# Kernel tuning notes

Hardware: AMD Instinct MI355X
Metric: run time of the kernel (lower is better)

Reference implementation:

```python
import jax, jax.numpy as jnp
import numpy as np

T, H, N, D = 4096, 16, 16, 64


def setup_inputs() -> dict:
    key = jax.random.key(0)
    ks = jax.random.split(key, 8)
    x = jax.random.normal(ks[0], (T, H, D), dtype=jnp.float32)
    dt = jax.random.uniform(ks[1], (T, H), dtype=jnp.float32) * 0.1  # small positive timesteps
    B = jax.random.normal(ks[2], (T, H, N), dtype=jnp.float32)
    C = jax.random.normal(ks[3], (T, H, N), dtype=jnp.float32)
    mask = jax.random.randint(ks[4], (T,), 0, 2).astype(jnp.float32)  # reset flags in {0,1}
    initial_carry = jax.random.normal(ks[5], (H, N, D), dtype=jnp.float32)
    log_decay = jax.random.normal(ks[6], (H,), dtype=jnp.float32) * 0.1
    skip_weight = jnp.ones((H, D), dtype=jnp.float32)
    return {"x": x, "dt": dt, "B": B, "C": C, "mask": mask,
            "initial_carry": initial_carry, "log_decay": log_decay,
            "skip_weight": skip_weight}


def _binary_operator(q_i, q_j):
    # elementwise; broadcasting replaces the original per-time vmap
    a_i, b_i, c_i = q_i
    a_j, b_j, c_j = q_j
    a_out = a_j * a_i * (1.0 - c_j) + a_j * c_j
    b_out = (a_j * b_i + b_j) * (1.0 - c_j) + b_j * c_j
    c_out = c_i * (1.0 - c_j) + c_j
    return (a_out, b_out, c_out)


def reference(x, dt, B, C, mask, initial_carry, log_decay, skip_weight):
    num_heads = dt.shape[1]
    decay_rate = -jnp.exp(log_decay)                        # [H]
    decay_factor = jnp.exp(dt * decay_rate[None, :])        # [T,H]
    decay_factor = decay_factor[:, :, None, None]           # [T,H,1,1]
    decay_factor = jnp.concatenate(
        [jnp.ones((1, num_heads, 1, 1), dtype=decay_factor.dtype), decay_factor], axis=0)
    driving_input = jnp.einsum('th,thn,thd->thnd', dt, B, x)  # [T,H,N,D]
    driving_input = jnp.concatenate([initial_carry[None, ...], driving_input], axis=0)
    m = jnp.concatenate([jnp.zeros((1,), dtype=mask.dtype), mask])
    m = m[:, None, None, None]                              # [T+1,1,1,1]
    _, hidden_states, _ = jax.lax.associative_scan(
        _binary_operator, (decay_factor, driving_input, m))
    next_carry = hidden_states[-1]                          # [H,N,D]
    valid_states = hidden_states[1:]                        # [T,H,N,D]
    output = jnp.einsum('thn,thnd->thd', C, valid_states)   # [T,H,D]
    output = output + skip_weight[None, :, :] * x
    return (next_carry, output)
```

## Files before the change

### kernel.cpp

```cpp
#include <hip/hip_runtime.h>

#define T_LEN 4096
#define H 16
#define N 16
#define D 64
#define NC 256
#define CL (T_LEN / NC)
#define HND (H * N * D)

static __device__ __forceinline__ unsigned short f2bf(float f) {
    union { float f; unsigned u; } v; v.f = f;
    unsigned r = (v.u + 0x7fffu + ((v.u >> 16) & 1u)) >> 16;
    return (unsigned short)r;
}
static __device__ __forceinline__ float bf2f(unsigned short s) {
    union { unsigned u; float f; } v; v.u = ((unsigned)s) << 16;
    return v.f;
}

__global__ __launch_bounds__(64)
void k1_local(const float* __restrict__ x, const float* __restrict__ dt,
              const float* __restrict__ B, const float* __restrict__ C,
              const float* __restrict__ mask, const float* __restrict__ log_decay,
              const float* __restrict__ skip_weight,
              unsigned short* __restrict__ Lb, float* __restrict__ Pbuf,
              float* __restrict__ OL) {
    const int c = blockIdx.x, h = blockIdx.y;
    const int d = threadIdx.x;
    const float rate = -__expf(log_decay[h]);
    const int t0 = c * CL;

    __shared__ float Bs[CL * N], Cs[CL * N];
    {
        const float4* Bg = (const float4*)B;
        const float4* Cg = (const float4*)C;
        const int j = d;
        const int row = j >> 2, off = j & 3;
        const float dtv = dt[(t0 + row) * H + h];
        float4 bv = Bg[((t0 + row) * H + h) * (N / 4) + off];
        bv.x *= dtv; bv.y *= dtv; bv.z *= dtv; bv.w *= dtv;
        ((float4*)Bs)[j] = bv;
        ((float4*)Cs)[j] = Cg[((t0 + row) * H + h) * (N / 4) + off];
    }
    __syncthreads();

    float s[N];
#pragma unroll
    for (int n = 0; n < N; ++n) s[n] = 0.f;
    const float swv = skip_weight[h * D + d];
    float P = 1.f;

#pragma unroll
    for (int ss = 0; ss < CL; ++ss) {
        const int t = t0 + ss;
        const float dtv = dt[t * H + h];
        const float mv  = mask[t];
        const float a   = (1.f - mv) * __expf(dtv * rate);
        const float xv  = x[(t * H + h) * D + d];
        P *= a;
        float acc = swv * xv;
        const float4* Br4 = (const float4*)(Bs + ss * N);
        const float4* Cr4 = (const float4*)(Cs + ss * N);
#pragma unroll
        for (int q = 0; q < 4; ++q) {
            const float4 bv = Br4[q];
            const float4 cv = Cr4[q];
            s[4*q+0] = a * s[4*q+0] + bv.x * xv;  acc += cv.x * s[4*q+0];
            s[4*q+1] = a * s[4*q+1] + bv.y * xv;  acc += cv.y * s[4*q+1];
            s[4*q+2] = a * s[4*q+2] + bv.z * xv;  acc += cv.z * s[4*q+2];
            s[4*q+3] = a * s[4*q+3] + bv.w * xv;  acc += cv.w * s[4*q+3];
        }
        OL[(t * H + h) * D + d] = acc;
    }

    unsigned short* Lp = Lb + ((size_t)(c * H + h) * N) * D + d;
#pragma unroll
    for (int n = 0; n < N; ++n) Lp[n * D] = f2bf(s[n]);
    if (d == 0) Pbuf[h * NC + c] = P;
}

__global__ __launch_bounds__(256)
void k2_combine(const float* __restrict__ initial_carry,
                unsigned short* __restrict__ LE, const float* __restrict__ Pbuf,
                float* __restrict__ next_carry) {
    const int idx = blockIdx.x * 256 + threadIdx.x;
    const int h = blockIdx.x >> 2;
    float carry = initial_carry[idx];

#pragma unroll 1
    for (int r = 0; r < NC / 128; ++r) {
        float l[128];
#pragma unroll
        for (int k = 0; k < 128; ++k)
            l[k] = bf2f(LE[(size_t)(r * 128 + k) * HND + idx]);
#pragma unroll
        for (int k = 0; k < 128; ++k) {
            const float p = Pbuf[h * NC + r * 128 + k];
            LE[(size_t)(r * 128 + k) * HND + idx] = f2bf(carry);
            carry = p * carry + l[k];
        }
    }
    next_carry[idx] = carry;
}

__global__ __launch_bounds__(64)
void k3_correct(const float* __restrict__ dt, const float* __restrict__ C,
                const float* __restrict__ mask, const float* __restrict__ log_decay,
                const unsigned short* __restrict__ Eb,
                const float* __restrict__ OL, float* __restrict__ out) {
    const int c = blockIdx.x, h = blockIdx.y;
    const int d = threadIdx.x;
    const float rate = -__expf(log_decay[h]);
    const int t0 = c * CL;

    __shared__ float Cs[CL * N];
    {
        const float4* Cg = (const float4*)C;
        const int j = d;
        const int row = j >> 2, off = j & 3;
        ((float4*)Cs)[j] = Cg[((t0 + row) * H + h) * (N / 4) + off];
    }
    __syncthreads();

    float E[N];
    {
        const unsigned short* Ep = Eb + ((size_t)(c * H + h) * N) * D + d;
#pragma unroll
        for (int n = 0; n < N; ++n) E[n] = bf2f(Ep[n * D]);
    }

    float pa = 1.f;
#pragma unroll
    for (int ss = 0; ss < CL; ++ss) {
        const int t = t0 + ss;
        const float dtv = dt[t * H + h];
        const float mv  = mask[t];
        pa *= (1.f - mv) * __expf(dtv * rate);
        const float4* Cr4 = (const float4*)(Cs + ss * N);
        float corr = 0.f;
#pragma unroll
        for (int q = 0; q < 4; ++q) {
            const float4 cv = Cr4[q];
            corr += cv.x * E[4*q+0] + cv.y * E[4*q+1]
                  + cv.z * E[4*q+2] + cv.w * E[4*q+3];
        }
        const float ol = OL[(t * H + h) * D + d];
        __builtin_nontemporal_store(ol + pa * corr, &out[(t * H + h) * D + d]);
    }
}

extern "C" void kernel_launch(void* const* d_in, const int* in_sizes, int n_in,
                              void* d_out, int out_size, void* d_ws, size_t ws_size,
                              hipStream_t stream) {
    const float* x    = (const float*)d_in[0];
    const float* dt   = (const float*)d_in[1];
    const float* B    = (const float*)d_in[2];
    const float* C    = (const float*)d_in[3];
    const float* mask = (const float*)d_in[4];
    const float* ic   = (const float*)d_in[5];
    const float* ld   = (const float*)d_in[6];
    const float* sw   = (const float*)d_in[7];
    float* out = (float*)d_out;

    float* Pbuf = (float*)d_ws;
    unsigned short* Lb = (unsigned short*)((char*)d_ws + 16384);
    float* OL = (float*)((char*)d_ws + 16384 + (size_t)NC * HND * 2);

    dim3 grid(NC, H), block(64);
    k1_local<<<grid, block, 0, stream>>>(x, dt, B, C, mask, ld, sw, Lb, Pbuf, OL);
    k2_combine<<<dim3(HND / 256), dim3(256), 0, stream>>>(ic, Lb, Pbuf, out);
    k3_correct<<<grid, block, 0, stream>>>(dt, C, mask, ld, Lb, OL, out + HND);
}
```

Before: 38.71 us.

## Recompute chunk scan from carried state instead of storing local outputs

The first pass now only computes each chunk's end state and decay product, and no longer writes the full local output array. The third kernel reruns the chunk recurrence starting from the combined carry-in state and produces the final output directly. This removes a large intermediate write plus a later read, at the cost of repeating the state recurrence arithmetic. It also packs four chunks per 256-thread block and precomputes the decay factors once into a workspace buffer that both kernels share.

New measurement: 35.49 us. -8.3%, faster.

```diff
diff --git a/kernel.cpp b/kernel.cpp
--- a/kernel.cpp
+++ b/kernel.cpp
@@ -6,6 +6,7 @@
 #define D 64
 #define NC 256
 #define CL (T_LEN / NC)
+#define CPB 4
 #define HND (H * N * D)
 
 static __device__ __forceinline__ unsigned short f2bf(float f) {
@@ -18,59 +19,58 @@
     return v.f;
 }
 
-__global__ __launch_bounds__(64)
+__global__ __launch_bounds__(256)
 void k1_local(const float* __restrict__ x, const float* __restrict__ dt,
-              const float* __restrict__ B, const float* __restrict__ C,
-              const float* __restrict__ mask, const float* __restrict__ log_decay,
-              const float* __restrict__ skip_weight,
+              const float* __restrict__ B, const float* __restrict__ mask,
+              const float* __restrict__ log_decay,
               unsigned short* __restrict__ Lb, float* __restrict__ Pbuf,
-              float* __restrict__ OL) {
-    const int c = blockIdx.x, h = blockIdx.y;
-    const int d = threadIdx.x;
+              float* __restrict__ Abuf) {
+    const int cq = blockIdx.x, h = blockIdx.y;
+    const int tid = threadIdx.x;
+    const int w = tid >> 6, d = tid & 63;
+    const int c = cq * CPB + w;
+    const int t00 = cq * CPB * CL;
     const float rate = -__expf(log_decay[h]);
-    const int t0 = c * CL;
 
-    __shared__ float Bs[CL * N], Cs[CL * N];
+    __shared__ float Bs[CPB * CL * N];
+    __shared__ float As[CPB * CL];
     {
         const float4* Bg = (const float4*)B;
-        const float4* Cg = (const float4*)C;
-        const int j = d;
+        const int j = tid;
         const int row = j >> 2, off = j & 3;
-        const float dtv = dt[(t0 + row) * H + h];
-        float4 bv = Bg[((t0 + row) * H + h) * (N / 4) + off];
+        const int t = t00 + row;
+        const float dtv = dt[t * H + h];
+        float4 bv = Bg[(t * H + h) * (N / 4) + off];
         bv.x *= dtv; bv.y *= dtv; bv.z *= dtv; bv.w *= dtv;
         ((float4*)Bs)[j] = bv;
-        ((float4*)Cs)[j] = Cg[((t0 + row) * H + h) * (N / 4) + off];
+        if (off == 0) {
+            const float av = (1.f - mask[t]) * __expf(dtv * rate);
+            As[row] = av;
+            Abuf[h * T_LEN + t] = av;
+        }
     }
     __syncthreads();
 
     float s[N];
 #pragma unroll
     for (int n = 0; n < N; ++n) s[n] = 0.f;
-    const float swv = skip_weight[h * D + d];
     float P = 1.f;
+    const int t0 = c * CL;
 
 #pragma unroll
     for (int ss = 0; ss < CL; ++ss) {
-        const int t = t0 + ss;
-        const float dtv = dt[t * H + h];
-        const float mv  = mask[t];
-        const float a   = (1.f - mv) * __expf(dtv * rate);
-        const float xv  = x[(t * H + h) * D + d];
+        const float a  = As[w * CL + ss];
+        const float xv = x[((t0 + ss) * H + h) * D + d];
         P *= a;
-        float acc = swv * xv;
-        const float4* Br4 = (const float4*)(Bs + ss * N);
-        const float4* Cr4 = (const float4*)(Cs + ss * N);
+        const float4* Br4 = (const float4*)(Bs + (w * CL + ss) * N);
 #pragma unroll
         for (int q = 0; q < 4; ++q) {
             const float4 bv = Br4[q];
-            const float4 cv = Cr4[q];
-            s[4*q+0] = a * s[4*q+0] + bv.x * xv;  acc += cv.x * s[4*q+0];
-            s[4*q+1] = a * s[4*q+1] + bv.y * xv;  acc += cv.y * s[4*q+1];
-            s[4*q+2] = a * s[4*q+2] + bv.z * xv;  acc += cv.z * s[4*q+2];
-            s[4*q+3] = a * s[4*q+3] + bv.w * xv;  acc += cv.w * s[4*q+3];
+            s[4*q+0] = a * s[4*q+0] + bv.x * xv;
+            s[4*q+1] = a * s[4*q+1] + bv.y * xv;
+            s[4*q+2] = a * s[4*q+2] + bv.z * xv;
+            s[4*q+3] = a * s[4*q+3] + bv.w * xv;
         }
-        OL[(t * H + h) * D + d] = acc;
     }
 
     unsigned short* Lp = Lb + ((size_t)(c * H + h) * N) * D + d;
@@ -103,49 +103,60 @@
     next_carry[idx] = carry;
 }
 
-__global__ __launch_bounds__(64)
-void k3_correct(const float* __restrict__ dt, const float* __restrict__ C,
-                const float* __restrict__ mask, const float* __restrict__ log_decay,
-                const unsigned short* __restrict__ Eb,
-                const float* __restrict__ OL, float* __restrict__ out) {
-    const int c = blockIdx.x, h = blockIdx.y;
-    const int d = threadIdx.x;
-    const float rate = -__expf(log_decay[h]);
-    const int t0 = c * CL;
+__global__ __launch_bounds__(256)
+void k3_scan(const float* __restrict__ x, const float* __restrict__ dt,
+             const float* __restrict__ B, const float* __restrict__ C,
+             const float* __restrict__ skip_weight,
+             const float* __restrict__ Abuf,
+             const unsigned short* __restrict__ Eb, float* __restrict__ out) {
+    const int cq = blockIdx.x, h = blockIdx.y;
+    const int tid = threadIdx.x;
+    const int w = tid >> 6, d = tid & 63;
+    const int c = cq * CPB + w;
+    const int t00 = cq * CPB * CL;
 
-    __shared__ float Cs[CL * N];
+    __shared__ float Bs[CPB * CL * N], Cs[CPB * CL * N];
+    __shared__ float As[CPB * CL];
     {
+        const float4* Bg = (const float4*)B;
         const float4* Cg = (const float4*)C;
-        const int j = d;
+        const int j = tid;
         const int row = j >> 2, off = j & 3;
-        ((float4*)Cs)[j] = Cg[((t0 + row) * H + h) * (N / 4) + off];
+        const int t = t00 + row;
+        const float dtv = dt[t * H + h];
+        float4 bv = Bg[(t * H + h) * (N / 4) + off];
+        bv.x *= dtv; bv.y *= dtv; bv.z *= dtv; bv.w *= dtv;
+        ((float4*)Bs)[j] = bv;
+        ((float4*)Cs)[j] = Cg[(t * H + h) * (N / 4) + off];
+        if (tid < CPB * CL) As[tid] = Abuf[h * T_LEN + t00 + tid];
     }
     __syncthreads();
 
-    float E[N];
-    {
-        const unsigned short* Ep = Eb + ((size_t)(c * H + h) * N) * D + d;
+    float s[N];
+    const unsigned short* Ep = Eb + ((size_t)(c * H + h) * N) * D + d;
 #pragma unroll
-        for (int n = 0; n < N; ++n) E[n] = bf2f(Ep[n * D]);
-    }
+    for (int n = 0; n < N; ++n) s[n] = bf2f(Ep[n * D]);
 
-    float pa = 1.f;
+    const float swv = skip_weight[h * D + d];
+    const int t0 = c * CL;
 #pragma unroll
     for (int ss = 0; ss < CL; ++ss) {
         const int t = t0 + ss;
-        const float dtv = dt[t * H + h];
-        const float mv  = mask[t];
-        pa *= (1.f - mv) * __expf(dtv * rate);
-        const float4* Cr4 = (const float4*)(Cs + ss * N);
-        float corr = 0.f;
+        const float a  = As[w * CL + ss];
+        const float xv = x[(t * H + h) * D + d];
+        float acc = swv * xv;
+        const float4* Br4 = (const float4*)(Bs + (w * CL + ss) * N);
+        const float4* Cr4 = (const float4*)(Cs + (w * CL + ss) * N);
 #pragma unroll
         for (int q = 0; q < 4; ++q) {
+            const float4 bv = Br4[q];
             const float4 cv = Cr4[q];
-            corr += cv.x * E[4*q+0] + cv.y * E[4*q+1]
-                  + cv.z * E[4*q+2] + cv.w * E[4*q+3];
+            s[4*q+0] = a * s[4*q+0] + bv.x * xv;  acc += cv.x * s[4*q+0];
+            s[4*q+1] = a * s[4*q+1] + bv.y * xv;  acc += cv.y * s[4*q+1];
+            s[4*q+2] = a * s[4*q+2] + bv.z * xv;  acc += cv.z * s[4*q+2];
+            s[4*q+3] = a * s[4*q+3] + bv.w * xv;  acc += cv.w * s[4*q+3];
         }
-        const float ol = OL[(t * H + h) * D + d];
-        __builtin_nontemporal_store(ol + pa * corr, &out[(t * H + h) * D + d]);
+        __builtin_nontemporal_store(acc, &out[(t * H + h) * D + d]);
     }
 }
 
@@ -163,11 +174,11 @@
     float* out = (float*)d_out;
 
     float* Pbuf = (float*)d_ws;
-    unsigned short* Lb = (unsigned short*)((char*)d_ws + 16384);
-    float* OL = (float*)((char*)d_ws + 16384 + (size_t)NC * HND * 2);
+    float* Abuf = (float*)((char*)d_ws + 16384);
+    unsigned short* Lb = (unsigned short*)((char*)d_ws + 16384 + T_LEN * H * 4);
 
-    dim3 grid(NC, H), block(64);
-    k1_local<<<grid, block, 0, stream>>>(x, dt, B, C, mask, ld, sw, Lb, Pbuf, OL);
+    dim3 grid(NC / CPB, H), block(256);
+    k1_local<<<grid, block, 0, stream>>>(x, dt, B, mask, ld, Lb, Pbuf, Abuf);
     k2_combine<<<dim3(HND / 256), dim3(256), 0, stream>>>(ic, Lb, Pbuf, out);
-    k3_correct<<<grid, block, 0, stream>>>(dt, C, mask, ld, Lb, OL, out + HND);
+    k3_scan<<<grid, block, 0, stream>>>(x, dt, B, C, sw, Abuf, Lb, out + HND);
 }
```
